# Kernel optimization log

Hardware: AMD Instinct MI355X
Metric: run time of the kernel (lower is better)

Reference implementation:

```python
import jax, jax.numpy as jnp
import numpy as np

NUM_HEADS = 8
D_MODEL = 512
D_Q = D_MODEL // NUM_HEADS
B, S = 4, 2048


def setup_inputs() -> dict:
    key = jax.random.key(0)
    ks = jax.random.split(key, 7)
    bound = 1.0 / np.sqrt(D_MODEL)  # kaiming_uniform with a=sqrt(5) on fan_in=d_model
    return {
        "x_query": jax.random.normal(ks[0], (B, S, D_MODEL), dtype=jnp.float32),
        "x_key": jax.random.normal(ks[1], (B, S, D_MODEL), dtype=jnp.float32),
        "x_value": jax.random.normal(ks[2], (B, S, D_MODEL), dtype=jnp.float32),
        "Q": jax.random.uniform(ks[3], (NUM_HEADS, D_MODEL, D_Q), minval=-bound, maxval=bound, dtype=jnp.float32),
        "K": jax.random.uniform(ks[4], (NUM_HEADS, D_MODEL, D_Q), minval=-bound, maxval=bound, dtype=jnp.float32),
        "V": jax.random.uniform(ks[5], (NUM_HEADS, D_MODEL, D_Q), minval=-bound, maxval=bound, dtype=jnp.float32),
        "Wout": jax.random.uniform(ks[6], (D_MODEL, D_MODEL), minval=-bound, maxval=bound, dtype=jnp.float32),
    }


def reference(x_query, x_key, x_value, Q, K, V, Wout):
    # per-head projections: [B,S,d_model] x [H,d_model,d_q] -> [B,H,S,d_q]
    q = jnp.einsum('bsd,hdq->bhsq', x_query, Q)
    k = jnp.einsum('bsd,hdq->bhsq', x_key, K)
    v = jnp.einsum('bsd,hdq->bhsq', x_value, V)
    scale = 1.0 / jnp.sqrt(jnp.asarray(q.shape[-1], q.dtype))
    scores = jnp.einsum('bhsq,bhtq->bhst', q, k) * scale  # [B,H,S,S]
    attn = jax.nn.softmax(scores, axis=-1)
    heads = jnp.einsum('bhst,bhtq->bhsq', attn, v)  # [B,H,S,d_q]
    # faithful to original: .view(B, S, -1) on [B,H,S,d_q] layout (no transpose)
    concat = heads.reshape(heads.shape[0], heads.shape[2], -1)
    return concat @ Wout.T
```

## Files before the change

### kernel.cpp

```cpp
#include <hip/hip_runtime.h>
#include <math.h>

#define BATCH 4
#define SEQ   2048
#define DM    512
#define NH    8
#define DQ    64
#define BS    (BATCH*SEQ)
#define BPAD  72

typedef short  short8  __attribute__((ext_vector_type(8)));
typedef float  floatx4 __attribute__((ext_vector_type(4)));
typedef unsigned short ushort8 __attribute__((ext_vector_type(8)));

__device__ __forceinline__ unsigned short f2bf(float f) {
    unsigned u = __float_as_uint(f);
    unsigned r = (u + 0x7fffu + ((u >> 16) & 1u)) >> 16;
    return (unsigned short)r;
}

__device__ __forceinline__ void async_copy16(const void* g, void* l) {
    __builtin_amdgcn_global_load_lds(
        (const __attribute__((address_space(1))) unsigned int*)g,
        (__attribute__((address_space(3))) unsigned int*)l, 16, 0, 0);
}

__global__ __launch_bounds__(256) void convert_x_kernel(
    const float* __restrict__ xq, const float* __restrict__ xk,
    const float* __restrict__ xv, unsigned short* __restrict__ xb)
{
    const float* X = (blockIdx.y == 0) ? xq : (blockIdx.y == 1) ? xk : xv;
    unsigned short* O = xb + (size_t)blockIdx.y * (BS * DM);
    const int i = (blockIdx.x * 256 + threadIdx.x) * 4;
    float4 v = *(const float4*)(X + i);
    ushort4 o;
    o.x = f2bf(v.x); o.y = f2bf(v.y); o.z = f2bf(v.z); o.w = f2bf(v.w);
    *(ushort4*)(O + i) = o;
}

__global__ __launch_bounds__(256) void convert_w_kernel(
    const float* __restrict__ Wq, const float* __restrict__ Wk,
    const float* __restrict__ Wv, const float* __restrict__ Wo,
    unsigned short* __restrict__ wt, unsigned short* __restrict__ wo)
{
    const int which = blockIdx.y;
    const int idx = blockIdx.x * 256 + threadIdx.x;
    if (which == 3) {
        float4 v = *(const float4*)(Wo + (size_t)idx * 4);
        ushort4 o;
        o.x = f2bf(v.x); o.y = f2bf(v.y); o.z = f2bf(v.z); o.w = f2bf(v.w);
        *(ushort4*)(wo + (size_t)idx * 4) = o;
    } else {
        const float* W = (which == 0) ? Wq : (which == 1) ? Wk : Wv;
        const int n   = idx >> 7;
        const int dd0 = (idx & 127) * 4;
        const int h = n >> 6, d = n & 63;
        ushort4 o;
        o.x = f2bf(W[((size_t)h * DM + dd0 + 0) * DQ + d]);
        o.y = f2bf(W[((size_t)h * DM + dd0 + 1) * DQ + d]);
        o.z = f2bf(W[((size_t)h * DM + dd0 + 2) * DQ + d]);
        o.w = f2bf(W[((size_t)h * DM + dd0 + 3) * DQ + d]);
        *(ushort4*)(wt + (size_t)which * (DM * DM) + (size_t)n * DM + dd0) = o;
    }
}

__global__ __launch_bounds__(256) void qkv_gemm_kernel(
    const unsigned short* __restrict__ xb, const unsigned short* __restrict__ wt,
    unsigned short* __restrict__ Oq, unsigned short* __restrict__ Ok,
    unsigned short* __restrict__ Ovt)
{
    __shared__ unsigned short As[128][64];
    __shared__ unsigned short Bs[128][64];

    const int which = blockIdx.z;
    const unsigned short* A  = xb + (size_t)which * (BS * DM);
    const unsigned short* Bt = wt + (size_t)which * (DM * DM);

    const int m0 = blockIdx.x * 128;
    const int n0 = blockIdx.y * 128;
    const int t = threadIdx.x, w = t >> 6, lane = t & 63;
    const int quad = lane >> 4, qr = lane & 15;
    const int lr = lane >> 3;
    const int lc = (lane & 7) * 8;
    const int mw = 64 * (w >> 1), nw = 64 * (w & 1);

    floatx4 acc[4][4] = {};

    for (int k0 = 0; k0 < DM; k0 += 64) {
        #pragma unroll
        for (int i = 0; i < 4; ++i) {
            const int row = i * 32 + w * 8;
            async_copy16(A  + (size_t)(m0 + row + lr) * DM + k0 + lc, &As[row][0]);
            async_copy16(Bt + (size_t)(n0 + row + lr) * DM + k0 + lc, &Bs[row][0]);
        }
        __syncthreads();
        #pragma unroll
        for (int kh = 0; kh < 2; ++kh) {
            short8 af[4], bf[4];
            #pragma unroll
            for (int si = 0; si < 4; ++si)
                af[si] = *(const short8*)&As[mw + 16 * si + qr][kh * 32 + quad * 8];
            #pragma unroll
            for (int sj = 0; sj < 4; ++sj)
                bf[sj] = *(const short8*)&Bs[nw + 16 * sj + qr][kh * 32 + quad * 8];
            #pragma unroll
            for (int si = 0; si < 4; ++si)
                #pragma unroll
                for (int sj = 0; sj < 4; ++sj)
                    acc[si][sj] = __builtin_amdgcn_mfma_f32_16x16x32_bf16(
                        af[si], bf[sj], acc[si][sj], 0, 0, 0);
        }
        __syncthreads();
    }

    const float osc = (which == 0) ? 0.125f : 1.0f;
    if (which < 2) {
        unsigned short* O = (which == 0) ? Oq : Ok;
        #pragma unroll
        for (int si = 0; si < 4; ++si) {
            #pragma unroll
            for (int sj = 0; sj < 4; ++sj) {
                const int col = n0 + nw + 16 * sj + qr;
                const int h = col >> 6, d = col & 63;
                #pragma unroll
                for (int r = 0; r < 4; ++r) {
                    const int row = m0 + mw + 16 * si + quad * 4 + r;
                    const int b = row >> 11, s = row & (SEQ - 1);
                    O[((size_t)(b * NH + h) * SEQ + s) * DQ + d] = f2bf(acc[si][sj][r] * osc);
                }
            }
        }
    } else {
        #pragma unroll
        for (int si = 0; si < 4; ++si) {
            #pragma unroll
            for (int sj = 0; sj < 4; ++sj) {
                const int col = n0 + nw + 16 * sj + qr;
                const int h = col >> 6, d = col & 63;
                #pragma unroll
                for (int r = 0; r < 4; ++r) {
                    const int row = m0 + mw + 16 * si + quad * 4 + r;
                    const int b = row >> 11, s = row & (SEQ - 1);
                    Ovt[((size_t)(b * NH + h) * DQ + d) * SEQ + s] = f2bf(acc[si][sj][r]);
                }
            }
        }
    }
}

__global__ __launch_bounds__(256) void out_gemm_kernel(
    const unsigned short* __restrict__ A, const unsigned short* __restrict__ Bt,
    float* __restrict__ C)
{
    __shared__ unsigned short As[128][64];
    __shared__ unsigned short Bs[128][64];

    const int m0 = blockIdx.x * 128;
    const int n0 = blockIdx.y * 128;
    const int t = threadIdx.x, w = t >> 6, lane = t & 63;
    const int quad = lane >> 4, qr = lane & 15;
    const int lr = lane >> 3;
    const int lc = (lane & 7) * 8;
    const int mw = 64 * (w >> 1), nw = 64 * (w & 1);

    floatx4 acc[4][4] = {};

    for (int k0 = 0; k0 < DM; k0 += 64) {
        #pragma unroll
        for (int i = 0; i < 4; ++i) {
            const int row = i * 32 + w * 8;
            async_copy16(A  + (size_t)(m0 + row + lr) * DM + k0 + lc, &As[row][0]);
            async_copy16(Bt + (size_t)(n0 + row + lr) * DM + k0 + lc, &Bs[row][0]);
        }
        __syncthreads();
        #pragma unroll
        for (int kh = 0; kh < 2; ++kh) {
            short8 af[4], bf[4];
            #pragma unroll
            for (int si = 0; si < 4; ++si)
                af[si] = *(const short8*)&As[mw + 16 * si + qr][kh * 32 + quad * 8];
            #pragma unroll
            for (int sj = 0; sj < 4; ++sj)
                bf[sj] = *(const short8*)&Bs[nw + 16 * sj + qr][kh * 32 + quad * 8];
            #pragma unroll
            for (int si = 0; si < 4; ++si)
                #pragma unroll
                for (int sj = 0; sj < 4; ++sj)
                    acc[si][sj] = __builtin_amdgcn_mfma_f32_16x16x32_bf16(
                        af[si], bf[sj], acc[si][sj], 0, 0, 0);
        }
        __syncthreads();
    }

    #pragma unroll
    for (int si = 0; si < 4; ++si) {
        #pragma unroll
        for (int sj = 0; sj < 4; ++sj) {
            const int col = n0 + nw + 16 * sj + qr;
            #pragma unroll
            for (int r = 0; r < 4; ++r) {
                const int row = m0 + mw + 16 * si + quad * 4 + r;
                C[(size_t)row * DM + col] = acc[si][sj][r];
            }
        }
    }
}

__global__ __launch_bounds__(256) void attn_kernel(
    const unsigned short* __restrict__ Qp, const unsigned short* __restrict__ Kp,
    const unsigned short* __restrict__ Vtp, unsigned short* __restrict__ Hd)
{
    __shared__ unsigned short Qs[64][BPAD];
    __shared__ unsigned short Ks[64][BPAD];
    __shared__ unsigned short Vts[64][BPAD];
    __shared__ unsigned short Ps[64][BPAD];

    const int s0 = blockIdx.x * 64;
    const int h  = blockIdx.y;
    const int b  = blockIdx.z;
    const size_t bh    = (size_t)(b * NH + h);
    const size_t base  = bh * SEQ * DQ;
    const size_t vbase = bh * DQ * SEQ;

    const int t    = threadIdx.x;
    const int w    = t >> 6;
    const int lane = t & 63;
    const int quad = lane >> 4;
    const int qr   = lane & 15;

    {
        const unsigned short* g = Qp + base + (size_t)s0 * DQ;
        #pragma unroll
        for (int i = 0; i < 2; ++i) {
            const int c = t + 256 * i;
            const int row = c >> 3, col8 = (c & 7) * 8;
            *(ushort8*)&Qs[row][col8] = *(const ushort8*)(g + row * DQ + col8);
        }
    }
    __syncthreads();
    const short8 aq0 = *(const short8*)&Qs[16 * w + qr][quad * 8];
    const short8 aq1 = *(const short8*)&Qs[16 * w + qr][quad * 8 + 32];

    floatx4 acc_o[4] = {};
    float l_lane = 0.f;

    ushort8 kreg[2], vreg[2];
    {
        const unsigned short* gk = Kp + base;
        const unsigned short* gv = Vtp + vbase;
        #pragma unroll
        for (int i = 0; i < 2; ++i) {
            const int c = t + 256 * i;
            const int row = c >> 3, col8 = (c & 7) * 8;
            kreg[i] = *(const ushort8*)(gk + row * DQ + col8);
            vreg[i] = *(const ushort8*)(gv + (size_t)row * SEQ + col8);
        }
    }

    for (int kt = 0; kt < SEQ; kt += 64) {
        __syncthreads();
        #pragma unroll
        for (int i = 0; i < 2; ++i) {
            const int c = t + 256 * i;
            const int row = c >> 3, col8 = (c & 7) * 8;
            *(ushort8*)&Ks[row][col8]  = kreg[i];
            *(ushort8*)&Vts[row][col8] = vreg[i];
        }
        __syncthreads();

        if (kt + 64 < SEQ) {
            const unsigned short* gk = Kp + base + (size_t)(kt + 64) * DQ;
            const unsigned short* gv = Vtp + vbase + (kt + 64);
            #pragma unroll
            for (int i = 0; i < 2; ++i) {
                const int c = t + 256 * i;
                const int row = c >> 3, col8 = (c & 7) * 8;
                kreg[i] = *(const ushort8*)(gk + row * DQ + col8);
                vreg[i] = *(const ushort8*)(gv + (size_t)row * SEQ + col8);
            }
        }

        #pragma unroll
        for (int si = 0; si < 4; ++si) {
            const short8 ak0 = *(const short8*)&Ks[16 * si + qr][quad * 8];
            const short8 ak1 = *(const short8*)&Ks[16 * si + qr][quad * 8 + 32];
            floatx4 z = {0.f, 0.f, 0.f, 0.f};
            z = __builtin_amdgcn_mfma_f32_16x16x32_bf16(ak0, aq0, z, 0, 0, 0);
            z = __builtin_amdgcn_mfma_f32_16x16x32_bf16(ak1, aq1, z, 0, 0, 0);
            const float p0 = __expf(z[0]), p1 = __expf(z[1]);
            const float p2 = __expf(z[2]), p3 = __expf(z[3]);
            l_lane += (p0 + p1) + (p2 + p3);
            ushort4 pk;
            pk.x = f2bf(p0); pk.y = f2bf(p1); pk.z = f2bf(p2); pk.w = f2bf(p3);
            *(ushort4*)&Ps[16 * w + qr][16 * si + quad * 4] = pk;
        }

        const short8 ap0 = *(const short8*)&Ps[16 * w + qr][quad * 8];
        const short8 ap1 = *(const short8*)&Ps[16 * w + qr][quad * 8 + 32];
        #pragma unroll
        for (int c = 0; c < 4; ++c) {
            const short8 bv0 = *(const short8*)&Vts[16 * c + qr][quad * 8];
            const short8 bv1 = *(const short8*)&Vts[16 * c + qr][quad * 8 + 32];
            acc_o[c] = __builtin_amdgcn_mfma_f32_16x16x32_bf16(ap0, bv0, acc_o[c], 0, 0, 0);
            acc_o[c] = __builtin_amdgcn_mfma_f32_16x16x32_bf16(ap1, bv1, acc_o[c], 0, 0, 0);
        }
    }

    l_lane += __shfl_xor(l_lane, 16);
    l_lane += __shfl_xor(l_lane, 32);
    float inv_l[4];
    #pragma unroll
    for (int r = 0; r < 4; ++r)
        inv_l[r] = 1.0f / __shfl(l_lane, quad * 4 + r);

    #pragma unroll
    for (int c = 0; c < 4; ++c)
        #pragma unroll
        for (int r = 0; r < 4; ++r)
            Hd[base + (size_t)(s0 + 16 * w + quad * 4 + r) * DQ + 16 * c + qr] =
                f2bf(acc_o[c][r] * inv_l[r]);
}

extern "C" void kernel_launch(void* const* d_in, const int* in_sizes, int n_in,
                              void* d_out, int out_size, void* d_ws, size_t ws_size,
                              hipStream_t stream) {
    const float* xq = (const float*)d_in[0];
    const float* xk = (const float*)d_in[1];
    const float* xv = (const float*)d_in[2];
    const float* Qw = (const float*)d_in[3];
    const float* Kw = (const float*)d_in[4];
    const float* Vw = (const float*)d_in[5];
    const float* Wo = (const float*)d_in[6];
    float* out = (float*)d_out;

    unsigned short* ws = (unsigned short*)d_ws;
    unsigned short* xb    = ws;
    unsigned short* wt    = ws + (size_t)12582912;
    unsigned short* wo    = ws + (size_t)13369344;
    unsigned short* q_ws  = ws + (size_t)13631488;
    unsigned short* k_ws  = ws + (size_t)17825792;
    unsigned short* vt_ws = ws + (size_t)22020096;
    unsigned short* h_ws  = ws + (size_t)26214400;

    convert_x_kernel<<<dim3(4096, 3), 256, 0, stream>>>(xq, xk, xv, xb);
    convert_w_kernel<<<dim3(256, 4), 256, 0, stream>>>(Qw, Kw, Vw, Wo, wt, wo);
    qkv_gemm_kernel<<<dim3(64, 4, 3), 256, 0, stream>>>(xb, wt, q_ws, k_ws, vt_ws);
    attn_kernel<<<dim3(SEQ / 64, NH, BATCH), 256, 0, stream>>>(q_ws, k_ws, vt_ws, h_ws);
    out_gemm_kernel<<<dim3(64, 4), 256, 0, stream>>>(h_ws, wo, out);
}
```

Before: 213.1 us.

## Fuse fp32-to-bf16 input conversion into QKV GEMM and use exp2 softmax

Removes the separate activation conversion kernel. The QKV GEMM now loads fp32 inputs directly, converts them in registers and stores bf16 into padded LDS, which avoids writing and re-reading a bf16 copy of all three inputs. The Q scale folds in log2(e) so attention can use exp2f instead of expf. bf16 rounding becomes round-half-up with a packed perm instruction. The trade-off is that each GEMM block now reads fp32 A tiles four times (once per N-tile block), losing the async LDS copy for A.

```diff
diff --git a/kernel.cpp b/kernel.cpp
--- a/kernel.cpp
+++ b/kernel.cpp
@@ -8,34 +8,27 @@
 #define DQ    64
 #define BS    (BATCH*SEQ)
 #define BPAD  72
+#define APAD  72
+
+#define QSCALE 0.18033688011112042f
 
 typedef short  short8  __attribute__((ext_vector_type(8)));
 typedef float  floatx4 __attribute__((ext_vector_type(4)));
 typedef unsigned short ushort8 __attribute__((ext_vector_type(8)));
 
 __device__ __forceinline__ unsigned short f2bf(float f) {
-    unsigned u = __float_as_uint(f);
-    unsigned r = (u + 0x7fffu + ((u >> 16) & 1u)) >> 16;
-    return (unsigned short)r;
+    return (unsigned short)((__float_as_uint(f) + 0x8000u) >> 16);
+}
+__device__ __forceinline__ unsigned pack2bf(float a, float b) {
+    unsigned ua = __float_as_uint(a) + 0x8000u;
+    unsigned ub = __float_as_uint(b) + 0x8000u;
+    return __builtin_amdgcn_perm(ub, ua, 0x07060302u);
 }
 
 __device__ __forceinline__ void async_copy16(const void* g, void* l) {
     __builtin_amdgcn_global_load_lds(
         (const __attribute__((address_space(1))) unsigned int*)g,
         (__attribute__((address_space(3))) unsigned int*)l, 16, 0, 0);
-}
-
-__global__ __launch_bounds__(256) void convert_x_kernel(
-    const float* __restrict__ xq, const float* __restrict__ xk,
-    const float* __restrict__ xv, unsigned short* __restrict__ xb)
-{
-    const float* X = (blockIdx.y == 0) ? xq : (blockIdx.y == 1) ? xk : xv;
-    unsigned short* O = xb + (size_t)blockIdx.y * (BS * DM);
-    const int i = (blockIdx.x * 256 + threadIdx.x) * 4;
-    float4 v = *(const float4*)(X + i);
-    ushort4 o;
-    o.x = f2bf(v.x); o.y = f2bf(v.y); o.z = f2bf(v.z); o.w = f2bf(v.w);
-    *(ushort4*)(O + i) = o;
 }
 
 __global__ __launch_bounds__(256) void convert_w_kernel(
@@ -47,33 +40,35 @@
     const int idx = blockIdx.x * 256 + threadIdx.x;
     if (which == 3) {
         float4 v = *(const float4*)(Wo + (size_t)idx * 4);
-        ushort4 o;
-        o.x = f2bf(v.x); o.y = f2bf(v.y); o.z = f2bf(v.z); o.w = f2bf(v.w);
-        *(ushort4*)(wo + (size_t)idx * 4) = o;
+        uint2 o;
+        o.x = pack2bf(v.x, v.y);
+        o.y = pack2bf(v.z, v.w);
+        *(uint2*)(wo + (size_t)idx * 4) = o;
     } else {
         const float* W = (which == 0) ? Wq : (which == 1) ? Wk : Wv;
         const int n   = idx >> 7;
         const int dd0 = (idx & 127) * 4;
         const int h = n >> 6, d = n & 63;
-        ushort4 o;
-        o.x = f2bf(W[((size_t)h * DM + dd0 + 0) * DQ + d]);
-        o.y = f2bf(W[((size_t)h * DM + dd0 + 1) * DQ + d]);
-        o.z = f2bf(W[((size_t)h * DM + dd0 + 2) * DQ + d]);
-        o.w = f2bf(W[((size_t)h * DM + dd0 + 3) * DQ + d]);
-        *(ushort4*)(wt + (size_t)which * (DM * DM) + (size_t)n * DM + dd0) = o;
+        uint2 o;
+        o.x = pack2bf(W[((size_t)h * DM + dd0 + 0) * DQ + d],
+                      W[((size_t)h * DM + dd0 + 1) * DQ + d]);
+        o.y = pack2bf(W[((size_t)h * DM + dd0 + 2) * DQ + d],
+                      W[((size_t)h * DM + dd0 + 3) * DQ + d]);
+        *(uint2*)(wt + (size_t)which * (DM * DM) + (size_t)n * DM + dd0) = o;
     }
 }
 
 __global__ __launch_bounds__(256) void qkv_gemm_kernel(
-    const unsigned short* __restrict__ xb, const unsigned short* __restrict__ wt,
+    const float* __restrict__ Xq, const float* __restrict__ Xk,
+    const float* __restrict__ Xv, const unsigned short* __restrict__ wt,
     unsigned short* __restrict__ Oq, unsigned short* __restrict__ Ok,
     unsigned short* __restrict__ Ovt)
 {
-    __shared__ unsigned short As[128][64];
+    __shared__ unsigned short As[128][APAD];
     __shared__ unsigned short Bs[128][64];
 
     const int which = blockIdx.z;
-    const unsigned short* A  = xb + (size_t)which * (BS * DM);
+    const float* X = (which == 0) ? Xq : (which == 1) ? Xk : Xv;
     const unsigned short* Bt = wt + (size_t)which * (DM * DM);
 
     const int m0 = blockIdx.x * 128;
@@ -82,6 +77,8 @@
     const int quad = lane >> 4, qr = lane & 15;
     const int lr = lane >> 3;
     const int lc = (lane & 7) * 8;
+    const int arow = t >> 4;
+    const int acol = (t & 15) * 4;
     const int mw = 64 * (w >> 1), nw = 64 * (w & 1);
 
     floatx4 acc[4][4] = {};
@@ -90,8 +87,16 @@
         #pragma unroll
         for (int i = 0; i < 4; ++i) {
             const int row = i * 32 + w * 8;
-            async_copy16(A  + (size_t)(m0 + row + lr) * DM + k0 + lc, &As[row][0]);
             async_copy16(Bt + (size_t)(n0 + row + lr) * DM + k0 + lc, &Bs[row][0]);
+        }
+        #pragma unroll
+        for (int i = 0; i < 8; ++i) {
+            const int row = i * 16 + arow;
+            float4 x4 = *(const float4*)(X + (size_t)(m0 + row) * DM + k0 + acol);
+            uint2 o;
+            o.x = pack2bf(x4.x, x4.y);
+            o.y = pack2bf(x4.z, x4.w);
+            *(uint2*)&As[row][acol] = o;
         }
         __syncthreads();
         #pragma unroll
@@ -113,7 +118,7 @@
         __syncthreads();
     }
 
-    const float osc = (which == 0) ? 0.125f : 1.0f;
+    const float osc = (which == 0) ? QSCALE : 1.0f;
     if (which < 2) {
         unsigned short* O = (which == 0) ? Oq : Ok;
         #pragma unroll
@@ -287,12 +292,13 @@
             floatx4 z = {0.f, 0.f, 0.f, 0.f};
             z = __builtin_amdgcn_mfma_f32_16x16x32_bf16(ak0, aq0, z, 0, 0, 0);
             z = __builtin_amdgcn_mfma_f32_16x16x32_bf16(ak1, aq1, z, 0, 0, 0);
-            const float p0 = __expf(z[0]), p1 = __expf(z[1]);
-            const float p2 = __expf(z[2]), p3 = __expf(z[3]);
+            const float p0 = exp2f(z[0]), p1 = exp2f(z[1]);
+            const float p2 = exp2f(z[2]), p3 = exp2f(z[3]);
             l_lane += (p0 + p1) + (p2 + p3);
-            ushort4 pk;
-            pk.x = f2bf(p0); pk.y = f2bf(p1); pk.z = f2bf(p2); pk.w = f2bf(p3);
-            *(ushort4*)&Ps[16 * w + qr][16 * si + quad * 4] = pk;
+            uint2 pk;
+            pk.x = pack2bf(p0, p1);
+            pk.y = pack2bf(p2, p3);
+            *(uint2*)&Ps[16 * w + qr][16 * si + quad * 4] = pk;
         }
 
         const short8 ap0 = *(const short8*)&Ps[16 * w + qr][quad * 8];
@@ -334,17 +340,15 @@
     float* out = (float*)d_out;
 
     unsigned short* ws = (unsigned short*)d_ws;
-    unsigned short* xb    = ws;
-    unsigned short* wt    = ws + (size_t)12582912;
-    unsigned short* wo    = ws + (size_t)13369344;
-    unsigned short* q_ws  = ws + (size_t)13631488;
-    unsigned short* k_ws  = ws + (size_t)17825792;
-    unsigned short* vt_ws = ws + (size_t)22020096;
-    unsigned short* h_ws  = ws + (size_t)26214400;
-
-    convert_x_kernel<<<dim3(4096, 3), 256, 0, stream>>>(xq, xk, xv, xb);
+    unsigned short* wt    = ws;
+    unsigned short* wo    = ws + (size_t)786432;
+    unsigned short* q_ws  = ws + (size_t)1048576;
+    unsigned short* k_ws  = ws + (size_t)5242880;
+    unsigned short* vt_ws = ws + (size_t)9437184;
+    unsigned short* h_ws  = ws + (size_t)13631488;
+
     convert_w_kernel<<<dim3(256, 4), 256, 0, stream>>>(Qw, Kw, Vw, Wo, wt, wo);
-    qkv_gemm_kernel<<<dim3(64, 4, 3), 256, 0, stream>>>(xb, wt, q_ws, k_ws, vt_ws);
+    qkv_gemm_kernel<<<dim3(64, 4, 3), 256, 0, stream>>>(xq, xk, xv, wt, q_ws, k_ws, vt_ws);
     attn_kernel<<<dim3(SEQ / 64, NH, BATCH), 256, 0, stream>>>(q_ws, k_ws, vt_ws, h_ws);
     out_gemm_kernel<<<dim3(64, 4), 256, 0, stream>>>(h_ws, wo, out);
 }
```

Result: no change. 215.2 us (+1.0%).
